# Optimization experiments

Hardware: AMD Instinct MI355X
Metric: run time of the kernel (lower is better)

Reference implementation:

```python
import jax, jax.numpy as jnp
import numpy as np

M_QAM = 16
LEAD_SYMBOLS = 20000  # pilot prefix in 'test' mode
NSYMB = 40000
NMODES = 256


def qam_constellation(M):
    # square M-QAM grid, normalized to unit average energy (constellation / sqrt(Es))
    m = int(np.sqrt(M))
    levels = 2 * np.arange(m) - (m - 1)
    c = (levels[:, None] + 1j * levels[None, :]).ravel()
    Es = np.mean(np.abs(c) ** 2)
    return (c / np.sqrt(Es)).astype(np.complex64)  # [M]


def setup_inputs() -> dict:
    key = jax.random.key(0)
    k = jax.random.split(key, 4)
    return {
        "Ei_real": jax.random.normal(k[0], (NSYMB, NMODES), jnp.float32),
        "Ei_imag": jax.random.normal(k[1], (NSYMB, NMODES), jnp.float32),
        "tx_real": jax.random.normal(k[2], (NSYMB, NMODES), jnp.float32),
        "tx_imag": jax.random.normal(k[3], (NSYMB, NMODES), jnp.float32),
        "eta": jnp.full((1,), 0.1, jnp.float32),  # learnable 'ddpll eta' param
    }


def _ddpll(Ei, symbTx, Kv, constSymb, mode):
    # k0,k1,k2 = 2*tanh(arctanh(0.5)), 2*tanh(arctanh(-0.5)), 2*tanh(arctanh(0.5))
    k0, k1, k2 = 1.0, -1.0, 1.0

    def Lk(phi, y, target, m):
        z = y * jnp.exp(1j * phi)
        dec = jnp.min(jnp.abs(z - constSymb) ** 2)  # decision-directed (min over M points)
        pil = jnp.abs(z - target) ** 2              # pilot-aided
        return dec * m + pil * (1.0 - m)

    g = jax.vmap(jax.grad(Lk, argnums=0))  # per-mode d Lk / d phi

    def step(carry, data):
        u, phi = carry                 # u: [3, Nmodes], phi: [Nmodes]
        xk, yk, mk = data              # [Nmodes] each
        gk = g(phi, yk, xk, mk)
        u1 = u[2]                      # u[1] <- old u[2]
        u0 = k0 * u[0] + k1 * u1 + k2 * gk  # momentum filter output
        new_u = jnp.stack([u0, u1, gk])
        return (new_u, phi - Kv * u0), phi  # emit pre-update phase (phip)

    Nmodes = Ei.shape[1]
    carry0 = (jnp.zeros((3, Nmodes), jnp.float32), jnp.zeros((Nmodes,), jnp.float32))
    _, theta = jax.lax.scan(step, carry0, (symbTx, Ei, mode))
    theta = jnp.unwrap(theta, axis=0, period=np.pi / 2)
    return Ei * jnp.exp(1j * theta), theta


def reference(Ei_real, Ei_imag, tx_real, tx_imag, eta):
    Ei = Ei_real + 1j * Ei_imag          # [Nsymb, Nmodes] complex64
    symbTx = tx_real + 1j * tx_imag
    Kv = jnp.tanh(eta[0])                # lr = tanh(eta)
    # mode: 0 on pilot rows (first lead_symbols in 'test' mode), 1 elsewhere
    mode = jnp.ones((NSYMB, NMODES), jnp.float32).at[:LEAD_SYMBOLS].set(0.0)
    constSymb = jnp.asarray(qam_constellation(M_QAM))
    Eo, theta = _ddpll(Ei, symbTx, Kv, constSymb, mode)
    return jnp.stack([Eo.real, Eo.imag], axis=-1), theta  # [Nsymb, Nmodes, 2], [Nsymb, Nmodes]
```

## Files before the change

### kernel.cpp

```cpp
#include <hip/hip_runtime.h>
#include <math.h>

#define NSYMB  40000
#define NMODES 256
#define LEAD   20000
#define UF     8

static __device__ __forceinline__ float crhypotf(float a, float b) {
    const double da = (double)a, db = (double)b;
    return (float)sqrt(da * da + db * db);
}

static __device__ __forceinline__ float fmod_p2_exact(float xf) {
    const double y  = (double)1.57079632679489661923f;
    const double ry = 1.0 / ((double)1.57079632679489661923f);
    const double ax = fabs((double)xf);
    const double q  = __builtin_trunc(ax * ry);
    double r = __builtin_fma(-q, y, ax);
    r = (r < 0.0) ? (r + y) : ((r >= y) ? (r - y) : r);
    return copysignf((float)r, xf);
}

static __device__ __forceinline__ void cr_sincosf_nb(double x, float& sf, float& cf) {
    const double invpio2 = 6.36619772367581382433e-01;
    const double pio2_1  = 1.57079632673412561417e+00;
    const double pio2_1t = 6.07710050650619224932e-11;
    const double fn = __builtin_rint(x * invpio2);
    const double rr = __builtin_fma(-fn, pio2_1, x);
    const double yy = rr - fn * pio2_1t;
    const double z  = yy * yy;
    double ps = __builtin_fma(z, 1.58969099521155010221e-10, -2.50507602534068634195e-08);
    ps = __builtin_fma(z, ps,  2.75573137070700676789e-06);
    ps = __builtin_fma(z, ps, -1.98412698298579493134e-04);
    ps = __builtin_fma(z, ps,  8.33333333332248946124e-03);
    ps = __builtin_fma(z, ps, -1.66666666666666324348e-01);
    const double sv = __builtin_fma(yy * z, ps, yy);
    double pc = __builtin_fma(z, -1.13596475577881948265e-11, 2.08757232129817482790e-09);
    pc = __builtin_fma(z, pc, -2.75573143513906633035e-07);
    pc = __builtin_fma(z, pc,  2.48015872894767294178e-05);
    pc = __builtin_fma(z, pc, -1.38888888888741095749e-03);
    pc = __builtin_fma(z, pc,  4.16666666666666019037e-02);
    const double hz = 0.5 * z;
    const double w1 = 1.0 - hz;
    const double cv = w1 + (((1.0 - w1) - hz) + z * (z * pc));
    const int n = ((int)fn) & 3;
    const float S = (float)sv, C = (float)cv;
    const bool sw = (n & 1) != 0;
    const float sa = sw ? C : S;
    const float ca = sw ? S : C;
    sf = (n & 2) ? -sa : sa;
    cf = ((n + 1) & 2) ? -ca : ca;
}

static __device__ __attribute__((noinline)) float2 dd_slow(float zre, float zim) {
#pragma clang fp contract(off)
    const double s10 = sqrt(10.0);
    float Lf[4];
    Lf[0] = (float)(-3.0 / s10); Lf[1] = (float)(-1.0 / s10);
    Lf[2] = (float)( 1.0 / s10); Lf[3] = (float)( 3.0 / s10);
    float dv[16], rv[16], wres[16], wims[16];
    float dmin = __builtin_inff();
#pragma unroll
    for (int k = 0; k < 16; ++k) {
        const float wre = zre - Lf[k >> 2];
        const float wim = zim - Lf[k & 3];
        const float r = crhypotf(wre, wim);
        const float d = r * r;
        wres[k] = wre; wims[k] = wim; rv[k] = r; dv[k] = d;
        dmin = fminf(dmin, d);
    }
    int cnt = 0;
#pragma unroll
    for (int k = 0; k < 16; ++k) cnt += (dv[k] == dmin) ? 1 : 0;
    float A, B;
    if (cnt == 1) {
        int j = 0;
#pragma unroll
        for (int k = 0; k < 16; ++k) if (dv[k] == dmin) j = k;
        A = 2.0f * wres[j];
        B = -(2.0f * wims[j]);
    } else {
        const float ctd = 1.0f / (float)cnt;
        float sa = 0.0f, sb = 0.0f;
#pragma unroll
        for (int k = 0; k < 16; ++k) {
            if (dv[k] == dmin) {
                const float ctr  = (2.0f * rv[k]) * ctd;
                const float ctm2 = ctr / rv[k];
                sa += (ctm2 * wres[k]);
                sb += -(ctm2 * wims[k]);
            }
        }
        A = sa; B = sb;
    }
    return make_float2(A, B);
}

template<bool PILOT>
static __device__ __forceinline__ void phi_step(
    float yre, float yim, float txr, float txi,
    float Kv, const float* Lf, float& phi)
{
#pragma clang fp contract(off)
    const float QTHf = 0.63245553203367588f;
    float s, c;
    cr_sincosf_nb((double)phi, s, c);
    const float zre = (yre * c) - (yim * s);
    const float zim = (yre * s) + (yim * c);
    float A, B;
    if (PILOT) {
        const float wre = zre - txr;
        const float wim = zim - txi;
        A = 2.0f * wre;
        B = -(2.0f * wim);
    } else {
        const float tr = (zre < 0.0f) ? ((zre < -QTHf) ? Lf[0] : Lf[1])
                                      : ((zre <  QTHf) ? Lf[2] : Lf[3]);
        const float ti = (zim < 0.0f) ? ((zim < -QTHf) ? Lf[0] : Lf[1])
                                      : ((zim <  QTHf) ? Lf[2] : Lf[3]);
        const float wre0 = zre - tr;
        const float wim0 = zim - ti;
        A = 2.0f * wre0;
        B = -(2.0f * wim0);
        const float ar = fabsf(zre), ai = fabsf(zim);
        const float mr = fminf(fabsf(ar - QTHf), ar);
        const float mi = fminf(fabsf(ai - QTHf), ai);
        const bool slow = !(mr > 1e-4f && mi > 1e-4f);
        if (__builtin_expect(__ballot(slow) != 0ULL, 0)) {
            if (slow) { const float2 ab = dd_slow(zre, zim); A = ab.x; B = ab.y; }
        }
    }
    const float ct_e_re = (A * yre) - (B * yim);
    const float ct_e_im = (A * yim) + (B * yre);
    const float ct_v_im = (ct_e_re * s) + (ct_e_im * c);
    const float gk = -ct_v_im;
    phi = phi - (Kv * gk);
}

__global__ __launch_bounds__(64)
void ddpll_seq(const float* __restrict__ ei_re,
               const float* __restrict__ ei_im,
               const float* __restrict__ tx_re,
               const float* __restrict__ tx_im,
               const float* __restrict__ eta,
               float* __restrict__ out)
{
#pragma clang fp contract(off)
    const int m = blockIdx.x * 64 + threadIdx.x;
    const float Kv = (float)tanh((double)eta[0]);

    const double s10 = sqrt(10.0);
    float Lf[4];
    Lf[0] = (float)(-3.0 / s10); Lf[1] = (float)(-1.0 / s10);
    Lf[2] = (float)( 1.0 / s10); Lf[3] = (float)( 3.0 / s10);

    float phi = 0.0f;
    float* __restrict__ th_out = out + (size_t)2 * NSYMB * NMODES;

    float pyr[UF], pyi[UF], pxr[UF], pxi[UF];
#pragma unroll
    for (int j = 0; j < UF; ++j) {
        const int idx = j * NMODES + m;
        pyr[j] = ei_re[idx]; pyi[j] = ei_im[idx];
        pxr[j] = tx_re[idx]; pxi[j] = tx_im[idx];
    }
    for (int tb = 0; tb < LEAD; tb += UF) {
        float yr[UF], yi[UF], xr[UF], xi[UF];
#pragma unroll
        for (int j = 0; j < UF; ++j) { yr[j]=pyr[j]; yi[j]=pyi[j]; xr[j]=pxr[j]; xi[j]=pxi[j]; }
        const int nb = tb + UF;
#pragma unroll
        for (int j = 0; j < UF; ++j) {
            const int idx = (nb + j) * NMODES + m;
            pyr[j] = ei_re[idx]; pyi[j] = ei_im[idx];
            pxr[j] = tx_re[idx]; pxi[j] = tx_im[idx];
        }
#pragma unroll
        for (int j = 0; j < UF; ++j) {
            th_out[(tb + j) * NMODES + m] = phi;
            phi_step<true>(yr[j], yi[j], xr[j], xi[j], Kv, Lf, phi);
        }
    }

#pragma unroll
    for (int j = 0; j < UF; ++j) {
        const int idx = (LEAD + j) * NMODES + m;
        pyr[j] = ei_re[idx]; pyi[j] = ei_im[idx];
    }
    for (int tb = LEAD; tb < NSYMB; tb += UF) {
        float yr[UF], yi[UF];
#pragma unroll
        for (int j = 0; j < UF; ++j) { yr[j]=pyr[j]; yi[j]=pyi[j]; }
        const int nb = tb + UF;
#pragma unroll
        for (int j = 0; j < UF; ++j) {
            const int tt = (nb + j < NSYMB) ? (nb + j) : (NSYMB - 1);
            const int idx = tt * NMODES + m;
            pyr[j] = ei_re[idx]; pyi[j] = ei_im[idx];
        }
#pragma unroll
        for (int j = 0; j < UF; ++j) {
            th_out[(tb + j) * NMODES + m] = phi;
            phi_step<false>(yr[j], yi[j], 0.0f, 0.0f, Kv, Lf, phi);
        }
    }
}

__global__ __launch_bounds__(256)
void ddpll_unwrapc(const float* __restrict__ th, float* __restrict__ c)
{
#pragma clang fp contract(off)
    const float P2f = 1.57079632679489661923f;
    const float P4f = 0.78539816339744830961f;
    const int idx = blockIdx.x * 256 + threadIdx.x;
    float cv = 0.0f;
    if (idx >= NMODES) {
        const float thv  = th[idx];
        const float prev = th[idx - NMODES];
        const float dd = thv - prev;
        float rm = fmod_p2_exact(dd + P4f);
        rm = (rm < 0.0f) ? rm + P2f : rm;
        float ddmod = rm - P4f;
        ddmod = (ddmod == -P4f && dd > 0.0f) ? P4f : ddmod;
        const bool take = !(fabsf(dd) < P4f);
        cv = take ? (ddmod - dd) : 0.0f;
    }
    c[idx] = cv;
}

__global__ __launch_bounds__(64)
void ddpll_scan(const float* __restrict__ c, float* __restrict__ th)
{
#pragma clang fp contract(off)
    const int m = blockIdx.x * 64 + threadIdx.x;
    float cum = 0.0f;
    float pc_[UF], pt_[UF];
#pragma unroll
    for (int j = 0; j < UF; ++j) {
        pc_[j] = c[j * NMODES + m];
        pt_[j] = th[j * NMODES + m];
    }
    for (int tb = 0; tb < NSYMB; tb += UF) {
        float cv[UF], tv[UF];
#pragma unroll
        for (int j = 0; j < UF; ++j) { cv[j]=pc_[j]; tv[j]=pt_[j]; }
        const int nb = tb + UF;
#pragma unroll
        for (int j = 0; j < UF; ++j) {
            const int tt = (nb + j < NSYMB) ? (nb + j) : (NSYMB - 1);
            pc_[j] = c[tt * NMODES + m];
            pt_[j] = th[tt * NMODES + m];
        }
#pragma unroll
        for (int j = 0; j < UF; ++j) {
            cum = cum + cv[j];
            th[(tb + j) * NMODES + m] = tv[j] + cum;
        }
    }
}

__global__ __launch_bounds__(256)
void ddpll_rot(const float* __restrict__ ei_re,
               const float* __restrict__ ei_im,
               float* __restrict__ out)
{
    const int idx = blockIdx.x * 256 + threadIdx.x;
    const float U = out[(size_t)2 * NSYMB * NMODES + idx];
    float su, cu;
    sincosf(U, &su, &cu);
    const float yre = ei_re[idx], yim = ei_im[idx];
    out[2 * idx]     = (yre * cu) - (yim * su);
    out[2 * idx + 1] = (yre * su) + (yim * cu);
}

extern "C" void kernel_launch(void* const* d_in, const int* in_sizes, int n_in,
                              void* d_out, int out_size, void* d_ws, size_t ws_size,
                              hipStream_t stream)
{
    (void)in_sizes; (void)n_in; (void)out_size; (void)d_ws; (void)ws_size;
    const float* ei_re = (const float*)d_in[0];
    const float* ei_im = (const float*)d_in[1];
    float* out = (float*)d_out;
    float* th  = out + (size_t)2 * NSYMB * NMODES;
    float* c   = out;

    ddpll_seq<<<dim3(NMODES / 64), dim3(64), 0, stream>>>(
        ei_re, ei_im,
        (const float*)d_in[2],
        (const float*)d_in[3],
        (const float*)d_in[4],
        out);
    ddpll_unwrapc<<<dim3(NSYMB * NMODES / 256), dim3(256), 0, stream>>>(th, c);
    ddpll_scan<<<dim3(NMODES / 64), dim3(64), 0, stream>>>(c, th);
    ddpll_rot<<<dim3(NSYMB * NMODES / 256), dim3(256), 0, stream>>>(
        ei_re, ei_im, out);
}
```

Baseline: 12.39 ms.

## Store intermediate phases mode-major so unwrap scan reads contiguous float4 runs

Result: faster. 11.88 ms (-4.1%).

```diff
diff --git a/kernel.cpp b/kernel.cpp
--- a/kernel.cpp
+++ b/kernel.cpp
@@ -5,6 +5,7 @@
 #define NMODES 256
 #define LEAD   20000
 #define UF     8
+#define NM     (NSYMB * NMODES)
 
 static __device__ __forceinline__ float crhypotf(float a, float b) {
     const double da = (double)a, db = (double)b;
@@ -155,7 +156,7 @@
     Lf[2] = (float)( 1.0 / s10); Lf[3] = (float)( 3.0 / s10);
 
     float phi = 0.0f;
-    float* __restrict__ th_out = out + (size_t)2 * NSYMB * NMODES;
+    float* __restrict__ th_p = out + (size_t)m * NSYMB;
 
     float pyr[UF], pyi[UF], pxr[UF], pxi[UF];
 #pragma unroll
@@ -177,7 +178,7 @@
         }
 #pragma unroll
         for (int j = 0; j < UF; ++j) {
-            th_out[(tb + j) * NMODES + m] = phi;
+            th_p[tb + j] = phi;
             phi_step<true>(yr[j], yi[j], xr[j], xi[j], Kv, Lf, phi);
         }
     }
@@ -200,23 +201,25 @@
         }
 #pragma unroll
         for (int j = 0; j < UF; ++j) {
-            th_out[(tb + j) * NMODES + m] = phi;
+            th_p[tb + j] = phi;
             phi_step<false>(yr[j], yi[j], 0.0f, 0.0f, Kv, Lf, phi);
         }
     }
 }
 
 __global__ __launch_bounds__(256)
-void ddpll_unwrapc(const float* __restrict__ th, float* __restrict__ c)
+void ddpll_unwrapc(const float* __restrict__ thT, float* __restrict__ cT)
 {
 #pragma clang fp contract(off)
     const float P2f = 1.57079632679489661923f;
     const float P4f = 0.78539816339744830961f;
-    const int idx = blockIdx.x * 256 + threadIdx.x;
+    const int g = blockIdx.x * 256 + threadIdx.x;
+    const int m = g / NSYMB;
+    const int t = g - m * NSYMB;
     float cv = 0.0f;
-    if (idx >= NMODES) {
-        const float thv  = th[idx];
-        const float prev = th[idx - NMODES];
+    if (t > 0) {
+        const float thv  = thT[g];
+        const float prev = thT[g - 1];
         const float dd = thv - prev;
         float rm = fmod_p2_exact(dd + P4f);
         rm = (rm < 0.0f) ? rm + P2f : rm;
@@ -225,36 +228,37 @@
         const bool take = !(fabsf(dd) < P4f);
         cv = take ? (ddmod - dd) : 0.0f;
     }
-    c[idx] = cv;
+    cT[g] = cv;
 }
 
 __global__ __launch_bounds__(64)
-void ddpll_scan(const float* __restrict__ c, float* __restrict__ th)
+void ddpll_scan(const float* __restrict__ thT, const float* __restrict__ cT,
+                float* __restrict__ theta)
 {
 #pragma clang fp contract(off)
     const int m = blockIdx.x * 64 + threadIdx.x;
+    const float4* __restrict__ pth = (const float4*)(thT + (size_t)m * NSYMB);
+    const float4* __restrict__ pcv = (const float4*)(cT  + (size_t)m * NSYMB);
     float cum = 0.0f;
-    float pc_[UF], pt_[UF];
-#pragma unroll
-    for (int j = 0; j < UF; ++j) {
-        pc_[j] = c[j * NMODES + m];
-        pt_[j] = th[j * NMODES + m];
-    }
-    for (int tb = 0; tb < NSYMB; tb += UF) {
-        float cv[UF], tv[UF];
-#pragma unroll
-        for (int j = 0; j < UF; ++j) { cv[j]=pc_[j]; tv[j]=pt_[j]; }
-        const int nb = tb + UF;
-#pragma unroll
-        for (int j = 0; j < UF; ++j) {
-            const int tt = (nb + j < NSYMB) ? (nb + j) : (NSYMB - 1);
-            pc_[j] = c[tt * NMODES + m];
-            pt_[j] = th[tt * NMODES + m];
-        }
-#pragma unroll
-        for (int j = 0; j < UF; ++j) {
-            cum = cum + cv[j];
-            th[(tb + j) * NMODES + m] = tv[j] + cum;
+    float4 bth[8], bcv[8];
+#pragma unroll
+    for (int j = 0; j < 8; ++j) { bth[j] = pth[j]; bcv[j] = pcv[j]; }
+    for (int tb = 0; tb < NSYMB; tb += 32) {
+        float4 th_[8], cv_[8];
+#pragma unroll
+        for (int j = 0; j < 8; ++j) { th_[j] = bth[j]; cv_[j] = bcv[j]; }
+        const int nb4 = (tb + 32) >> 2;
+#pragma unroll
+        for (int j = 0; j < 8; ++j) { bth[j] = pth[nb4 + j]; bcv[j] = pcv[nb4 + j]; }
+#pragma unroll
+        for (int j = 0; j < 8; ++j) {
+#pragma unroll
+            for (int k = 0; k < 4; ++k) {
+                const float cc = (&cv_[j].x)[k];
+                const float tt = (&th_[j].x)[k];
+                cum = cum + cc;
+                theta[(tb + j * 4 + k) * NMODES + m] = tt + cum;
+            }
         }
     }
 }
@@ -265,7 +269,7 @@
                float* __restrict__ out)
 {
     const int idx = blockIdx.x * 256 + threadIdx.x;
-    const float U = out[(size_t)2 * NSYMB * NMODES + idx];
+    const float U = out[(size_t)2 * NM + idx];
     float su, cu;
     sincosf(U, &su, &cu);
     const float yre = ei_re[idx], yim = ei_im[idx];
@@ -281,8 +285,9 @@
     const float* ei_re = (const float*)d_in[0];
     const float* ei_im = (const float*)d_in[1];
     float* out = (float*)d_out;
-    float* th  = out + (size_t)2 * NSYMB * NMODES;
-    float* c   = out;
+    float* thT = out;
+    float* cT  = out + (size_t)NM;
+    float* th  = out + (size_t)2 * NM;
 
     ddpll_seq<<<dim3(NMODES / 64), dim3(64), 0, stream>>>(
         ei_re, ei_im,
@@ -290,8 +295,7 @@
         (const float*)d_in[3],
         (const float*)d_in[4],
         out);
-    ddpll_unwrapc<<<dim3(NSYMB * NMODES / 256), dim3(256), 0, stream>>>(th, c);
-    ddpll_scan<<<dim3(NMODES / 64), dim3(64), 0, stream>>>(c, th);
-    ddpll_rot<<<dim3(NSYMB * NMODES / 256), dim3(256), 0, stream>>>(
-        ei_re, ei_im, out);
-}
+    ddpll_unwrapc<<<dim3(NM / 256), dim3(256), 0, stream>>>(thT, cT);
+    ddpll_scan<<<dim3(NMODES / 64), dim3(64), 0, stream>>>(thT, cT, th);
+    ddpll_rot<<<dim3(NM / 256), dim3(256), 0, stream>>>(ei_re, ei_im, out);
+}
```
